# Optimization experiments

Hardware: AMD Instinct MI355X
Metric: run time of the kernel (lower is better)

## Reference

```python
import jax, jax.numpy as jnp
import numpy as np

B, T, C, H = 2, 2048, 1024, 16
HD = C // H  # head dim = 64


def setup_inputs() -> dict:
    key = jax.random.key(0)
    k1, k2, k3 = jax.random.split(key, 3)
    scale_in = 1.0 / np.sqrt(C)
    x = jax.random.normal(k1, (B, T, C), dtype=jnp.float32)
    w_qkv = jax.random.normal(k2, (C, 3 * C), dtype=jnp.float32) * scale_in
    b_qkv = jnp.zeros((3 * C,), dtype=jnp.float32)
    w_out = jax.random.normal(k3, (C, C), dtype=jnp.float32) * scale_in
    b_out = jnp.zeros((C,), dtype=jnp.float32)
    return {"x": x, "w_qkv": w_qkv, "b_qkv": b_qkv, "w_out": w_out, "b_out": b_out}


def reference(x, w_qkv, b_qkv, w_out, b_out):
    Bq, Tq, Cq = x.shape
    qkv = x @ w_qkv + b_qkv                       # [B,T,3C]
    q, k, v = jnp.split(qkv, 3, axis=-1)          # each [B,T,C]
    # [B,T,C] -> [B,H,T,HD]
    q = q.reshape(Bq, Tq, H, HD).transpose(0, 2, 1, 3)
    k = k.reshape(Bq, Tq, H, HD).transpose(0, 2, 1, 3)
    v = v.reshape(Bq, Tq, H, HD).transpose(0, 2, 1, 3)
    scale = 1.0 / np.sqrt(HD)
    scores = jnp.einsum("bhqd,bhkd->bhqk", q, k) * scale  # [B,H,T,T]
    causal = jnp.tril(jnp.ones((Tq, Tq), dtype=bool))
    scores = jnp.where(causal[None, None], scores, jnp.finfo(scores.dtype).min)
    attn = jax.nn.softmax(scores, axis=-1)
    y = jnp.einsum("bhqk,bhkd->bhqd", attn, v)    # [B,H,T,HD]
    y = y.transpose(0, 2, 1, 3).reshape(Bq, Tq, Cq)
    return y @ w_out + b_out
```

## Files before the change

### kernel.cpp

```cpp
#include <hip/hip_runtime.h>
#include <hip/hip_bf16.h>


#define B_ 2
#define T_ 2048
#define C_ 1024
#define H_ 16
#define HD_ 64
#define M_ (B_ * T_)
#define N3_ (3 * C_)
#define QK2_ 2048
#define QSCALE 0.18033688f

typedef __attribute__((ext_vector_type(8))) short short8;
typedef __attribute__((ext_vector_type(4))) short short4v;
typedef __attribute__((ext_vector_type(4))) float floatx4;

__device__ __forceinline__ unsigned short f2b(float f) {
    __hip_bfloat16 h = __float2bfloat16(f);
    return *reinterpret_cast<unsigned short*>(&h);
}

__device__ __forceinline__ float fexp2(float x) {
#if __has_builtin(__builtin_amdgcn_exp2f)
    return __builtin_amdgcn_exp2f(x);
#else
    return exp2f(x);
#endif
}

__device__ __forceinline__ void glds16(const void* g, void* l) {
    __builtin_amdgcn_global_load_lds(
        (const __attribute__((address_space(1))) void*)g,
        (__attribute__((address_space(3))) void*)l, 16, 0, 0);
}

__global__ __launch_bounds__(256) void prep(
    const float* __restrict__ x, const float* __restrict__ w_qkv,
    const float* __restrict__ w_out, unsigned short* __restrict__ xb,
    unsigned short* __restrict__ wt1, unsigned short* __restrict__ wt2) {
    __shared__ float t[64][33];
    const int bi = blockIdx.x;
    const int tid = threadIdx.x;
    if (bi < 4096) {
        int i = (bi * 256 + tid) * 4;
        float4 v = *reinterpret_cast<const float4*>(x + i);
        short4v s;
        s[0] = (short)f2b(v.x); s[1] = (short)f2b(v.y);
        s[2] = (short)f2b(v.z); s[3] = (short)f2b(v.w);
        *reinterpret_cast<short4v*>(xb + i) = s;
        return;
    }
    const float* src; unsigned short* dst; int n0, k0, N;
    if (bi < 4096 + 1536) {
        int u = bi - 4096;
        src = w_qkv; dst = wt1; N = N3_;
        k0 = (u & 15) * 64; n0 = (u >> 4) * 32;
    } else {
        int u = bi - (4096 + 1536);
        src = w_out; dst = wt2; N = C_;
        k0 = (u & 15) * 64; n0 = (u >> 4) * 32;
    }
    const int tx = tid & 31, ty = tid >> 5;
#pragma unroll
    for (int i = 0; i < 8; i++)
        t[ty + i * 8][tx] = src[(size_t)(k0 + ty + i * 8) * N + n0 + tx];
    __syncthreads();
    const int row = tid >> 3;
    const int kp  = (tid & 7) * 8;
    short8 o;
#pragma unroll
    for (int j = 0; j < 8; j++) o[j] = (short)f2b(t[kp + j][row]);
    *reinterpret_cast<short8*>(&dst[(size_t)(n0 + row) * C_ + k0 + kp]) = o;
}

template<int EPI, int BN>
__global__ __launch_bounds__(256) void gemm_glds(
    const unsigned short* __restrict__ A, const unsigned short* __restrict__ Bt,
    const float* __restrict__ bias, void* __restrict__ Cp,
    unsigned short* __restrict__ vtp, int M, int N, int K) {
    constexpr int NI = BN / 32;
    __shared__ __align__(16) unsigned short Al[128 * 64];
    __shared__ __align__(16) unsigned short Bl[BN * 64];

    const int tid  = threadIdx.x;
    const int lane = tid & 63;
    const int w    = tid >> 6;
    const int c16  = lane & 15;
    const int quad = lane >> 4;
    const int NT  = N / BN;
    const int pe  = NT >> 3;
    const int xcd = blockIdx.x & 7;
    const int ii  = blockIdx.x >> 3;
    const int n0  = (xcd * pe + ii % pe) * BN;
    const int m0  = (ii / pe) * 128;
    const int wm = (w >> 1) * 64;
    const int wn = (w & 1) * (BN / 2);

    floatx4 acc[4][NI] = {};

    const int srow = lane >> 3;
    const int sch  = ((lane & 7) ^ srow) * 8;
    const unsigned short* ag = A + (size_t)(m0 + w * 32 + srow) * K + sch;
    const unsigned short* bg = Bt + (size_t)(n0 + w * (BN / 4) + srow) * K + sch;

    const int s7 = c16 & 7;

    for (int k0 = 0; k0 < K; k0 += 64) {
        __syncthreads();
#pragma unroll
        for (int i = 0; i < 4; i++)
            glds16(ag + k0 + (size_t)(i * 8) * K, &Al[(w * 32 + i * 8) * 64]);
#pragma unroll
        for (int i = 0; i < BN / 32; i++)
            glds16(bg + k0 + (size_t)(i * 8) * K,
                   &Bl[(w * (BN / 4) + i * 8) * 64]);
        __syncthreads();

        short8 af[4][2], bf[NI][2];
#pragma unroll
        for (int im = 0; im < 4; im++)
#pragma unroll
            for (int kk = 0; kk < 2; kk++)
                af[im][kk] = *reinterpret_cast<const short8*>(
                    &Al[(wm + im * 16 + c16) * 64 + ((kk * 4 + quad) ^ s7) * 8]);
#pragma unroll
        for (int in = 0; in < NI; in++)
#pragma unroll
            for (int kk = 0; kk < 2; kk++)
                bf[in][kk] = *reinterpret_cast<const short8*>(
                    &Bl[(wn + in * 16 + c16) * 64 + ((kk * 4 + quad) ^ s7) * 8]);
#pragma unroll
        for (int im = 0; im < 4; im++)
#pragma unroll
            for (int in = 0; in < NI; in++)
#pragma unroll
                for (int kk = 0; kk < 2; kk++)
                    acc[im][in] = __builtin_amdgcn_mfma_f32_16x16x32_bf16(
                        af[im][kk], bf[in][kk], acc[im][in], 0, 0, 0);
    }

    const int ncol = n0 + wn;
    float bv[NI];
#pragma unroll
    for (int in = 0; in < NI; in++) bv[in] = bias[ncol + in * 16 + c16];

    if (EPI == 0) {
        float* C = (float*)Cp;
#pragma unroll
        for (int im = 0; im < 4; im++)
#pragma unroll
            for (int r = 0; r < 4; r++) {
                int row = m0 + wm + im * 16 + quad * 4 + r;
#pragma unroll
                for (int in = 0; in < NI; in++)
                    C[(size_t)row * N + ncol + in * 16 + c16] =
                        acc[im][in][r] + bv[in];
            }
    } else {
        if (ncol < 2 * C_) {
            const float fac = (ncol < C_) ? QSCALE : 1.0f;
            unsigned short* qkp = (unsigned short*)Cp;
#pragma unroll
            for (int im = 0; im < 4; im++)
#pragma unroll
                for (int r = 0; r < 4; r++) {
                    int row = m0 + wm + im * 16 + quad * 4 + r;
#pragma unroll
                    for (int in = 0; in < NI; in++)
                        qkp[(size_t)row * QK2_ + ncol + in * 16 + c16] =
                            f2b((acc[im][in][r] + bv[in]) * fac);
                }
        } else {
#pragma unroll
            for (int im = 0; im < 4; im++) {
                int row0 = m0 + wm + im * 16 + quad * 4;
                int b  = row0 >> 11;
                int t0 = row0 & (T_ - 1);
#pragma unroll
                for (int in = 0; in < NI; in++) {
                    int dfull = ncol - 2 * C_ + in * 16 + c16;
                    short4v sv;
#pragma unroll
                    for (int r = 0; r < 4; r++)
                        sv[r] = (short)f2b(acc[im][in][r] + bv[in]);
                    *reinterpret_cast<short4v*>(
                        &vtp[(((size_t)(b << 10) + dfull) << 11) + t0]) = sv;
                }
            }
        }
    }
}

#define ATTN_CHUNK(MASKED, Kb, Vb, kb)                                        \
{                                                                             \
    const int sxr = c16 & 7;                                                  \
    const int ch0 = (quad ^ sxr) * 8;                                         \
    const int ch1 = ((4 + quad) ^ sxr) * 8;                                   \
    const int kr0 = (ws * 32 + c16) * 64;                                     \
    const int kr1 = (ws * 32 + 16 + c16) * 64;                                \
    short8 kf00 = *reinterpret_cast<const short8*>(&(Kb)[kr0 + ch0]);         \
    short8 kf01 = *reinterpret_cast<const short8*>(&(Kb)[kr0 + ch1]);         \
    short8 kf10 = *reinterpret_cast<const short8*>(&(Kb)[kr1 + ch0]);         \
    short8 kf11 = *reinterpret_cast<const short8*>(&(Kb)[kr1 + ch1]);         \
    short8 pf[2];                                                             \
    _Pragma("unroll")                                                         \
    for (int qt = 0; qt < 2; qt++) {                                          \
        floatx4 s0 = __builtin_amdgcn_mfma_f32_16x16x32_bf16(                 \
            kf00, af[qt][0], z, 0, 0, 0);                                     \
        s0 = __builtin_amdgcn_mfma_f32_16x16x32_bf16(                         \
            kf01, af[qt][1], s0, 0, 0, 0);                                    \
        floatx4 s1 = __builtin_amdgcn_mfma_f32_16x16x32_bf16(                 \
            kf10, af[qt][0], z, 0, 0, 0);                                     \
        s1 = __builtin_amdgcn_mfma_f32_16x16x32_bf16(                         \
            kf11, af[qt][1], s1, 0, 0, 0);                                    \
        float ll = 0.f;                                                       \
        short8 p8;                                                            \
        _Pragma("unroll")                                                     \
        for (int r = 0; r < 4; r++) {                                         \
            float p0, p1;                                                     \
            if (MASKED) {                                                     \
                int key0 = (kb) + ws * 32 + quad * 4 + r;                     \
                int qr = q0 + wq * 32 + qt * 16 + c16;                        \
                p0 = (key0 <= qr) ? fexp2(s0[r]) : 0.f;                       \
                p1 = (key0 + 16 <= qr) ? fexp2(s1[r]) : 0.f;                  \
            } else {                                                          \
                p0 = fexp2(s0[r]);                                            \
                p1 = fexp2(s1[r]);                                            \
            }                                                                 \
            ll += p0 + p1;                                                    \
            p8[r] = (short)f2b(p0);                                           \
            p8[4 + r] = (short)f2b(p1);                                       \
        }                                                                     \
        lacc[qt] += ll;                                                       \
        pf[qt] = p8;                                                          \
    }                                                                         \
    _Pragma("unroll")                                                         \
    for (int dt = 0; dt < 4; dt++) {                                          \
        const int vr = (dt * 16 + c16) * 64;                                  \
        short4v v0 = *reinterpret_cast<const short4v*>(                       \
            &(Vb)[vr + (((ws * 4 + (quad >> 1)) ^ sxr) << 3) + (quad & 1) * 4]); \
        short4v v1 = *reinterpret_cast<const short4v*>(                       \
            &(Vb)[vr + (((ws * 4 + 2 + (quad >> 1)) ^ sxr) << 3) + (quad & 1) * 4]); \
        short8 vv;                                                            \
        vv[0] = v0[0]; vv[1] = v0[1]; vv[2] = v0[2]; vv[3] = v0[3];           \
        vv[4] = v1[0]; vv[5] = v1[1]; vv[6] = v1[2]; vv[7] = v1[3];           \
        _Pragma("unroll")                                                     \
        for (int qt = 0; qt < 2; qt++)                                        \
            O[qt][dt] = __builtin_amdgcn_mfma_f32_16x16x32_bf16(              \
                pf[qt], vv, O[qt][dt], 0, 0, 0);                              \
    }                                                                         \
}

__global__ __launch_bounds__(256, 3) void attn_mfma(
    const unsigned short* __restrict__ qk,
    const unsigned short* __restrict__ vt,
    unsigned short* __restrict__ y) {
    __shared__ __align__(16) unsigned short Kl[2][64 * 64];
    __shared__ __align__(16) unsigned short Vl[2][64 * 64];

    const int tid  = threadIdx.x;
    const int lane = tid & 63;
    const int w    = tid >> 6;
    const int wq   = w & 1;
    const int ws   = w >> 1;
    const int c16  = lane & 15;
    const int quad = lane >> 4;
    const int bh = blockIdx.x & 31;
    const int t  = 31 - (blockIdx.x >> 5);
    const int b  = bh >> 4;
    const int h  = bh & 15;
    const int q0 = t * 64;
    const int nch = t + 1;

    const unsigned short* qrow = qk + (size_t)b * T_ * QK2_ + h * HD_;
    const unsigned short* krow = qrow + C_;
    const unsigned short* vrow = vt + ((size_t)bh << 6) * T_;

    short8 af[2][2];
#pragma unroll
    for (int qt = 0; qt < 2; qt++)
#pragma unroll
        for (int hh = 0; hh < 2; hh++)
            af[qt][hh] = *reinterpret_cast<const short8*>(
                qrow + (size_t)(q0 + wq * 32 + qt * 16 + c16) * QK2_ +
                hh * 32 + quad * 8);

    floatx4 O[2][4] = {};
    float lacc[2] = {0.f, 0.f};
    const floatx4 z = {0.f, 0.f, 0.f, 0.f};

    const int r8 = lane >> 3;
    const int sw = ((lane & 7) ^ r8) * 8;

#pragma unroll
    for (int i = 0; i < 2; i++) {
        glds16(krow + (size_t)(w * 16 + i * 8 + r8) * QK2_ + sw,
               &Kl[0][(w * 16 + i * 8) * 64]);
        glds16(vrow + (size_t)(w * 16 + i * 8 + r8) * T_ + sw,
               &Vl[0][(w * 16 + i * 8) * 64]);
    }

    for (int c = 0; c < nch; c++) {
        __syncthreads();
        if (c + 1 < nch) {
            const int kb2 = (c + 1) * 64;
            const int nb = (c + 1) & 1;
#pragma unroll
            for (int i = 0; i < 2; i++) {
                glds16(krow + (size_t)(kb2 + w * 16 + i * 8 + r8) * QK2_ + sw,
                       &Kl[nb][(w * 16 + i * 8) * 64]);
                glds16(vrow + (size_t)(w * 16 + i * 8 + r8) * T_ + kb2 + sw,
                       &Vl[nb][(w * 16 + i * 8) * 64]);
            }
        }
        const int kb = c * 64;
        const unsigned short* Kb = Kl[c & 1];
        const unsigned short* Vb = Vl[c & 1];
        if (c + 1 < nch) {
            ATTN_CHUNK(0, Kb, Vb, kb)
        } else if (!(wq == 0 && ws == 1)) {
            ATTN_CHUNK(1, Kb, Vb, kb)
        }
    }

    __syncthreads();
    float* Of = (float*)&Kl[0][0];
    float* Lb = (float*)&Vl[0][0];
    if (ws) {
#pragma unroll
        for (int qt = 0; qt < 2; qt++) {
#pragma unroll
            for (int dt = 0; dt < 4; dt++)
                *reinterpret_cast<floatx4*>(
                    &Of[wq * 2048 + qt * 1024 + dt * 256 + lane * 4]) = O[qt][dt];
            Lb[wq * 128 + qt * 64 + lane] = lacc[qt];
        }
    }
    __syncthreads();
    if (ws == 0) {
#pragma unroll
        for (int qt = 0; qt < 2; qt++) {
#pragma unroll
            for (int dt = 0; dt < 4; dt++)
                O[qt][dt] += *reinterpret_cast<const floatx4*>(
                    &Of[wq * 2048 + qt * 1024 + dt * 256 + lane * 4]);
            float lj = lacc[qt] + Lb[wq * 128 + qt * 64 + lane];
            lj += __shfl_xor(lj, 16);
            lj += __shfl_xor(lj, 32);
            float lr[4];
#pragma unroll
            for (int r = 0; r < 4; r++)
                lr[r] = __shfl(lj, quad * 4 + r);

#pragma unroll
            for (int dt = 0; dt < 4; dt++)
#pragma unroll
                for (int r = 0; r < 4; r++) {
                    float val = O[qt][dt][r] / fmaxf(lr[r], 1e-30f);
                    y[((size_t)b * T_ + q0 + wq * 32 + qt * 16 + quad * 4 + r)
                          * C_ + h * HD_ + dt * 16 + c16] = f2b(val);
                }
        }
    }
}

extern "C" void kernel_launch(void* const* d_in, const int* in_sizes, int n_in,
                              void* d_out, int out_size, void* d_ws, size_t ws_size,
                              hipStream_t stream) {
    const float* x     = (const float*)d_in[0];
    const float* w_qkv = (const float*)d_in[1];
    const float* b_qkv = (const float*)d_in[2];
    const float* w_out = (const float*)d_in[3];
    const float* b_out = (const float*)d_in[4];
    float* out = (float*)d_out;

    unsigned short* qkb = (unsigned short*)d_ws;
    unsigned short* vtb = qkb + (size_t)M_ * QK2_;
    unsigned short* yb  = vtb + (size_t)B_ * H_ * HD_ * T_;
    unsigned short* wt1 = yb + (size_t)M_ * C_;
    unsigned short* wt2 = wt1 + (size_t)N3_ * C_;
    unsigned short* xb  = wt2 + (size_t)C_ * C_;

    prep<<<4096 + 1536 + 512, 256, 0, stream>>>(x, w_qkv, w_out, xb, wt1, wt2);

    gemm_glds<1, 128><<<(N3_ / 128) * (M_ / 128), 256, 0, stream>>>(
        xb, wt1, b_qkv, qkb, vtb, M_, N3_, C_);

    attn_mfma<<<B_ * H_ * 32, 256, 0, stream>>>(qkb, vtb, yb);

    gemm_glds<0, 64><<<(C_ / 64) * (M_ / 128), 256, 0, stream>>>(
        yb, wt2, b_out, out, nullptr, M_, C_, C_);
}
```

Before: 170.6 us.

## Load K/V fragments directly from global memory and compute row sums via MFMA

Removes the LDS double-buffered K/V staging and per-chunk barriers, so each wave loads its K and V MFMA fragments straight from global memory (relying on cache). The softmax denominator is now computed with an extra MFMA against a ones vector instead of scalar adds and shuffles. This drops the sync overhead and shuffle reduction but duplicates global loads across waves that share K/V, and the V loads become small strided reads.

```diff
diff --git a/kernel.cpp b/kernel.cpp
--- a/kernel.cpp
+++ b/kernel.cpp
@@ -192,17 +192,25 @@
     }
 }
 
-#define ATTN_CHUNK(MASKED, Kb, Vb, kb)                                        \
+#define ATTN_CHUNK(MASKED, kb)                                                \
 {                                                                             \
-    const int sxr = c16 & 7;                                                  \
-    const int ch0 = (quad ^ sxr) * 8;                                         \
-    const int ch1 = ((4 + quad) ^ sxr) * 8;                                   \
-    const int kr0 = (ws * 32 + c16) * 64;                                     \
-    const int kr1 = (ws * 32 + 16 + c16) * 64;                                \
-    short8 kf00 = *reinterpret_cast<const short8*>(&(Kb)[kr0 + ch0]);         \
-    short8 kf01 = *reinterpret_cast<const short8*>(&(Kb)[kr0 + ch1]);         \
-    short8 kf10 = *reinterpret_cast<const short8*>(&(Kb)[kr1 + ch0]);         \
-    short8 kf11 = *reinterpret_cast<const short8*>(&(Kb)[kr1 + ch1]);         \
+    const unsigned short* kb0 = krow + (size_t)((kb) + ws * 32 + c16) * QK2_; \
+    short8 kf00 = *reinterpret_cast<const short8*>(kb0 + quad * 8);           \
+    short8 kf01 = *reinterpret_cast<const short8*>(kb0 + 32 + quad * 8);      \
+    short8 kf10 = *reinterpret_cast<const short8*>(kb0 + 16 * QK2_ + quad * 8); \
+    short8 kf11 = *reinterpret_cast<const short8*>(kb0 + 16 * QK2_ + 32 + quad * 8); \
+    short8 vf[4];                                                             \
+    _Pragma("unroll")                                                         \
+    for (int dt = 0; dt < 4; dt++) {                                          \
+        const unsigned short* vb = vrow + (size_t)(dt * 16 + c16) * T_ +      \
+                                   (kb) + ws * 32 + quad * 4;                 \
+        short4v v0 = *reinterpret_cast<const short4v*>(vb);                   \
+        short4v v1 = *reinterpret_cast<const short4v*>(vb + 16);              \
+        short8 vv;                                                            \
+        vv[0] = v0[0]; vv[1] = v0[1]; vv[2] = v0[2]; vv[3] = v0[3];           \
+        vv[4] = v1[0]; vv[5] = v1[1]; vv[6] = v1[2]; vv[7] = v1[3];           \
+        vf[dt] = vv;                                                          \
+    }                                                                         \
     short8 pf[2];                                                             \
     _Pragma("unroll")                                                         \
     for (int qt = 0; qt < 2; qt++) {                                          \
@@ -214,7 +222,6 @@
             kf10, af[qt][0], z, 0, 0, 0);                                     \
         s1 = __builtin_amdgcn_mfma_f32_16x16x32_bf16(                         \
             kf11, af[qt][1], s1, 0, 0, 0);                                    \
-        float ll = 0.f;                                                       \
         short8 p8;                                                            \
         _Pragma("unroll")                                                     \
         for (int r = 0; r < 4; r++) {                                         \
@@ -228,36 +235,29 @@
                 p0 = fexp2(s0[r]);                                            \
                 p1 = fexp2(s1[r]);                                            \
             }                                                                 \
-            ll += p0 + p1;                                                    \
             p8[r] = (short)f2b(p0);                                           \
             p8[4 + r] = (short)f2b(p1);                                       \
         }                                                                     \
-        lacc[qt] += ll;                                                       \
         pf[qt] = p8;                                                          \
     }                                                                         \
     _Pragma("unroll")                                                         \
-    for (int dt = 0; dt < 4; dt++) {                                          \
-        const int vr = (dt * 16 + c16) * 64;                                  \
-        short4v v0 = *reinterpret_cast<const short4v*>(                       \
-            &(Vb)[vr + (((ws * 4 + (quad >> 1)) ^ sxr) << 3) + (quad & 1) * 4]); \
-        short4v v1 = *reinterpret_cast<const short4v*>(                       \
-            &(Vb)[vr + (((ws * 4 + 2 + (quad >> 1)) ^ sxr) << 3) + (quad & 1) * 4]); \
-        short8 vv;                                                            \
-        vv[0] = v0[0]; vv[1] = v0[1]; vv[2] = v0[2]; vv[3] = v0[3];           \
-        vv[4] = v1[0]; vv[5] = v1[1]; vv[6] = v1[2]; vv[7] = v1[3];           \
+    for (int qt = 0; qt < 2; qt++)                                            \
+        O1[qt] = __builtin_amdgcn_mfma_f32_16x16x32_bf16(                     \
+            pf[qt], ones, O1[qt], 0, 0, 0);                                   \
+    _Pragma("unroll")                                                         \
+    for (int dt = 0; dt < 4; dt++)                                            \
         _Pragma("unroll")                                                     \
         for (int qt = 0; qt < 2; qt++)                                        \
             O[qt][dt] = __builtin_amdgcn_mfma_f32_16x16x32_bf16(              \
-                pf[qt], vv, O[qt][dt], 0, 0, 0);                              \
-    }                                                                         \
+                pf[qt], vf[dt], O[qt][dt], 0, 0, 0);                          \
 }
 
 __global__ __launch_bounds__(256, 3) void attn_mfma(
     const unsigned short* __restrict__ qk,
     const unsigned short* __restrict__ vt,
     unsigned short* __restrict__ y) {
-    __shared__ __align__(16) unsigned short Kl[2][64 * 64];
-    __shared__ __align__(16) unsigned short Vl[2][64 * 64];
+    __shared__ __align__(16) float Of[4096];
+    __shared__ __align__(16) float Lb[1024];
 
     const int tid  = threadIdx.x;
     const int lane = tid & 63;
@@ -287,46 +287,22 @@
                 hh * 32 + quad * 8);
 
     floatx4 O[2][4] = {};
-    float lacc[2] = {0.f, 0.f};
+    floatx4 O1[2] = {};
+    float lacc_unused = 0.f; (void)lacc_unused;
     const floatx4 z = {0.f, 0.f, 0.f, 0.f};
-
-    const int r8 = lane >> 3;
-    const int sw = ((lane & 7) ^ r8) * 8;
-
-#pragma unroll
-    for (int i = 0; i < 2; i++) {
-        glds16(krow + (size_t)(w * 16 + i * 8 + r8) * QK2_ + sw,
-               &Kl[0][(w * 16 + i * 8) * 64]);
-        glds16(vrow + (size_t)(w * 16 + i * 8 + r8) * T_ + sw,
-               &Vl[0][(w * 16 + i * 8) * 64]);
-    }
+    short8 ones;
+#pragma unroll
+    for (int j = 0; j < 8; j++) ones[j] = (short)0x3F80;
 
     for (int c = 0; c < nch; c++) {
-        __syncthreads();
+        const int kb = c * 64;
         if (c + 1 < nch) {
-            const int kb2 = (c + 1) * 64;
-            const int nb = (c + 1) & 1;
-#pragma unroll
-            for (int i = 0; i < 2; i++) {
-                glds16(krow + (size_t)(kb2 + w * 16 + i * 8 + r8) * QK2_ + sw,
-                       &Kl[nb][(w * 16 + i * 8) * 64]);
-                glds16(vrow + (size_t)(w * 16 + i * 8 + r8) * T_ + kb2 + sw,
-                       &Vl[nb][(w * 16 + i * 8) * 64]);
-            }
+            ATTN_CHUNK(0, kb)
+        } else if (!(wq == 0 && ws == 1)) {
+            ATTN_CHUNK(1, kb)
         }
-        const int kb = c * 64;
-        const unsigned short* Kb = Kl[c & 1];
-        const unsigned short* Vb = Vl[c & 1];
-        if (c + 1 < nch) {
-            ATTN_CHUNK(0, Kb, Vb, kb)
-        } else if (!(wq == 0 && ws == 1)) {
-            ATTN_CHUNK(1, Kb, Vb, kb)
-        }
-    }
-
-    __syncthreads();
-    float* Of = (float*)&Kl[0][0];
-    float* Lb = (float*)&Vl[0][0];
+    }
+
     if (ws) {
 #pragma unroll
         for (int qt = 0; qt < 2; qt++) {
@@ -334,7 +310,8 @@
             for (int dt = 0; dt < 4; dt++)
                 *reinterpret_cast<floatx4*>(
                     &Of[wq * 2048 + qt * 1024 + dt * 256 + lane * 4]) = O[qt][dt];
-            Lb[wq * 128 + qt * 64 + lane] = lacc[qt];
+            *reinterpret_cast<floatx4*>(
+                &Lb[wq * 512 + qt * 256 + lane * 4]) = O1[qt];
         }
     }
     __syncthreads();
@@ -345,13 +322,8 @@
             for (int dt = 0; dt < 4; dt++)
                 O[qt][dt] += *reinterpret_cast<const floatx4*>(
                     &Of[wq * 2048 + qt * 1024 + dt * 256 + lane * 4]);
-            float lj = lacc[qt] + Lb[wq * 128 + qt * 64 + lane];
-            lj += __shfl_xor(lj, 16);
-            lj += __shfl_xor(lj, 32);
-            float lr[4];
-#pragma unroll
-            for (int r = 0; r < 4; r++)
-                lr[r] = __shfl(lj, quad * 4 + r);
+            floatx4 lr = O1[qt] + *reinterpret_cast<const floatx4*>(
+                    &Lb[wq * 512 + qt * 256 + lane * 4]);
 
 #pragma unroll
             for (int dt = 0; dt < 4; dt++)
```

New measurement: 246.1 us. 1.44x slower.
